# Kernel tuning notes

Hardware: AMD Instinct MI355X
Metric: run time of the kernel (lower is better)

The kernel has to match this reference:

```python
import jax, jax.numpy as jnp
import numpy as np

N = 50000      # nodes
E = 800000     # edges (before self loops)
ND = 64        # node_dim
ED = 32        # embed_dim
D = ND + 2 * ED  # 128, EGNN working feature dim


def _mlp2(x, w1, b1, w2, b2):
    return jax.nn.relu(x @ w1 + b1) @ w2 + b2


def _egnn_layer(x, pos, src, dst, nm_w1, nm_b1, nm_w2, nm_b2,
                cm_w1, cm_b1, cm_w2, cm_b2):
    # x_i = x[dst] (target), x_j = x[src] (source); aggregate at dst (PyG 'add')
    edge_vec = pos[src] - pos[dst]                                   # pos_j - pos_i, [E+N, 3]
    dist = jnp.sqrt(jnp.sum(edge_vec * edge_vec, axis=-1, keepdims=True) + 1e-8)
    h = jnp.concatenate([x[dst], x[src], dist], axis=-1)             # [E+N, 2D+1]
    edge_msg = _mlp2(h, nm_w1, nm_b1, nm_w2, nm_b2)                  # [E+N, D]
    coord_upd = _mlp2(dist, cm_w1, cm_b1, cm_w2, cm_b2) * edge_vec   # [E+N, 3]
    x_out = x + jax.ops.segment_sum(edge_msg, dst, num_segments=N)
    pos_out = pos + jax.ops.segment_sum(coord_upd, dst, num_segments=N)
    return x_out, pos_out


def setup_inputs() -> dict:
    key = jax.random.key(0)
    ks = jax.random.split(key, 24)

    def p(k, shape, scale=0.02):
        return (jax.random.normal(k, shape, jnp.float32) * scale)

    inp = {
        'x_t': jax.random.normal(ks[0], (N, ND), jnp.float32),
        'pos': jax.random.normal(ks[1], (N, 3), jnp.float32),
        'edge_index': jax.random.randint(ks[2], (2, E), 0, N, dtype=jnp.int32),
        't': jax.random.randint(ks[3], (1,), 0, 1000, dtype=jnp.int32),
        'cond_embed': jax.random.normal(ks[4], (1, ED), jnp.float32),
        # time embedding: Linear(1,32) -> ReLU -> Linear(32, ED)
        'te_w1': p(ks[5], (1, 32)), 'te_b1': jnp.zeros((32,), jnp.float32),
        'te_w2': p(ks[6], (32, ED)), 'te_b2': jnp.zeros((ED,), jnp.float32),
        # EGNN layer 1
        'l1_nm_w1': p(ks[7], (2 * D + 1, 128)), 'l1_nm_b1': jnp.zeros((128,), jnp.float32),
        'l1_nm_w2': p(ks[8], (128, D)), 'l1_nm_b2': jnp.zeros((D,), jnp.float32),
        'l1_cm_w1': p(ks[9], (1, 128)), 'l1_cm_b1': jnp.zeros((128,), jnp.float32),
        'l1_cm_w2': p(ks[10], (128, 1)), 'l1_cm_b2': jnp.zeros((1,), jnp.float32),
        # EGNN layer 2
        'l2_nm_w1': p(ks[11], (2 * D + 1, 128)), 'l2_nm_b1': jnp.zeros((128,), jnp.float32),
        'l2_nm_w2': p(ks[12], (128, D)), 'l2_nm_b2': jnp.zeros((D,), jnp.float32),
        'l2_cm_w1': p(ks[13], (1, 128)), 'l2_cm_b1': jnp.zeros((128,), jnp.float32),
        'l2_cm_w2': p(ks[14], (128, 1)), 'l2_cm_b2': jnp.zeros((1,), jnp.float32),
        # bond predictor: Linear(2D,64) -> ReLU -> Linear(64,4)
        'bp_w1': p(ks[15], (2 * D, 64)), 'bp_b1': jnp.zeros((64,), jnp.float32),
        'bp_w2': p(ks[16], (64, 4)), 'bp_b2': jnp.zeros((4,), jnp.float32),
    }
    return inp


def reference(x_t, pos, edge_index, t, cond_embed,
              te_w1, te_b1, te_w2, te_b2,
              l1_nm_w1, l1_nm_b1, l1_nm_w2, l1_nm_b2,
              l1_cm_w1, l1_cm_b1, l1_cm_w2, l1_cm_b2,
              l2_nm_w1, l2_nm_b1, l2_nm_w2, l2_nm_b2,
              l2_cm_w1, l2_cm_b1, l2_cm_w2, l2_cm_b2,
              bp_w1, bp_b1, bp_w2, bp_b2):
    n = x_t.shape[0]
    # time embedding, broadcast over nodes
    t_in = (t.reshape(-1, 1).astype(jnp.float32)) / 1000.0
    t_embed = _mlp2(t_in, te_w1, te_b1, te_w2, te_b2)            # [1, ED]
    x_input = jnp.concatenate([
        x_t,
        jnp.broadcast_to(cond_embed, (n, cond_embed.shape[-1])),
        jnp.broadcast_to(t_embed, (n, t_embed.shape[-1])),
    ], axis=1)                                                    # [N, D]

    # add self loops (appended, as in PyG add_self_loops)
    loop = jnp.arange(n, dtype=edge_index.dtype)
    src = jnp.concatenate([edge_index[0], loop])
    dst = jnp.concatenate([edge_index[1], loop])

    x1, pos1 = _egnn_layer(x_input, pos, src, dst,
                           l1_nm_w1, l1_nm_b1, l1_nm_w2, l1_nm_b2,
                           l1_cm_w1, l1_cm_b1, l1_cm_w2, l1_cm_b2)
    x2, pos2 = _egnn_layer(x1, pos1, src, dst,
                           l2_nm_w1, l2_nm_b1, l2_nm_w2, l2_nm_b2,
                           l2_cm_w1, l2_cm_b1, l2_cm_w2, l2_cm_b2)

    edge_feats = jnp.concatenate([x2[edge_index[0]], x2[edge_index[1]]], axis=1)  # [E, 2D]
    bond_logits = _mlp2(edge_feats, bp_w1, bp_b1, bp_w2, bp_b2)                   # [E, 4]
    return (x2[:, :x_t.shape[1]], bond_logits)
```

## Files before the change

### kernel.cpp

```cpp
#include <hip/hip_runtime.h>
#include <hip/hip_bf16.h>
#include <stdint.h>

typedef float  f32x4 __attribute__((ext_vector_type(4)));
typedef short  s16x8 __attribute__((ext_vector_type(8)));
typedef unsigned short u16x8 __attribute__((ext_vector_type(8)));
typedef unsigned short ushort_t;

__device__ __forceinline__ short f2bf(float f) {
  union { float f; unsigned u; } x; x.f = f;
  unsigned r = x.u + 0x7fffu + ((x.u >> 16) & 1u);
  return (short)(r >> 16);
}
__device__ __forceinline__ float bf2f(unsigned short u) {
  union { unsigned u; float f; } x; x.u = ((unsigned)u) << 16; return x.f;
}
__device__ __forceinline__ float i2f(int v) {
  union { int i; float f; } x; x.i = v; return x.f;
}
__device__ __forceinline__ int f2i(float v) {
  union { float f; int i; } x; x.f = v; return x.i;
}

__device__ __forceinline__ void pack_one(const float* W, int cols, int local, short* dst) {
  int NT = cols / 16;
  int j = local & 7, l = (local >> 3) & 63;
  int nt = (local >> 9) % NT;
  int kt = (local >> 9) / NT;
  int k = kt * 32 + ((l >> 4) * 8) + j;
  int ncol = nt * 16 + (l & 15);
  dst[local] = f2bf(W[(size_t)k * cols + ncol]);
}

__global__ __launch_bounds__(256)
void k_front(const float* __restrict__ w0, const float* __restrict__ w1,
             const float* __restrict__ w2, const float* __restrict__ w3,
             const float* __restrict__ w4, const float* __restrict__ w5,
             const float* __restrict__ w6, const float* __restrict__ w7,
             short* __restrict__ out,
             const int* __restrict__ t, const float* __restrict__ tw1,
             const float* __restrict__ tb1, const float* __restrict__ tw2,
             const float* __restrict__ tb2,
             const float* __restrict__ xt, const float* __restrict__ cond,
             ushort_t* __restrict__ X, int n,
             const int* __restrict__ edst, int E, int* __restrict__ deg,
             int nbBuild) {
  int b = blockIdx.x;
  if (b < 448) {
    int i = b * 256 + threadIdx.x;
    if (i < 98304) {
      int r = i >> 14, local = i & 16383;
      const float* W = r == 0 ? w0 : r == 1 ? w1 : r == 2 ? w2 : r == 3 ? w3 : r == 4 ? w4 : w5;
      pack_one(W, 128, local, out + r * 16384);
    } else {
      int j = i - 98304;
      int r = j >> 13, local = j & 8191;
      pack_one(r ? w7 : w6, 64, local, out + 98304 + r * 8192);
    }
    return;
  }
  b -= 448;
  if (b < nbBuild) {
    __shared__ float h[32], tembL[32];
    int j = threadIdx.x;
    if (j < 32) h[j] = fmaxf(((float)t[0] / 1000.0f) * tw1[j] + tb1[j], 0.f);
    __syncthreads();
    if (j < 32) {
      float acc = tb2[j];
      for (int k2 = 0; k2 < 32; ++k2) acc += h[k2] * tw2[k2 * 32 + j];
      tembL[j] = acc;
    }
    __syncthreads();
    int i = b * 256 + threadIdx.x;
    if (i >= n * 16) return;
    int node = i >> 4, c8 = i & 15;
    float va[8];
    if (c8 < 8)       { const float* p = &xt[(size_t)node * 64 + c8 * 8];
                        #pragma unroll
                        for (int q = 0; q < 8; ++q) va[q] = p[q]; }
    else if (c8 < 12) { const float* p = &cond[(c8 - 8) * 8];
                        #pragma unroll
                        for (int q = 0; q < 8; ++q) va[q] = p[q]; }
    else              { const float* p = &tembL[(c8 - 12) * 8];
                        #pragma unroll
                        for (int q = 0; q < 8; ++q) va[q] = p[q]; }
    u16x8 o;
    #pragma unroll
    for (int q = 0; q < 8; ++q) o[q] = f2bf(va[q]);
    *(u16x8*)&X[(size_t)node * 128 + c8 * 8] = o;
    return;
  }
  b -= nbBuild;
  int e = b * 256 + threadIdx.x;
  if (e < E) atomicAdd(&deg[edst[e]], 1);
}

__global__ void k_scan1(const int* __restrict__ deg, int* __restrict__ tmp,
                        int* __restrict__ bsum, int n) {
  __shared__ int sh[256];
  int i = blockIdx.x * 256 + threadIdx.x;
  int v = (i < n) ? deg[i] + 1 : 0;
  sh[threadIdx.x] = v; __syncthreads();
  for (int off = 1; off < 256; off <<= 1) {
    int t = (threadIdx.x >= off) ? sh[threadIdx.x - off] : 0;
    __syncthreads();
    sh[threadIdx.x] += t;
    __syncthreads();
  }
  if (i < n) tmp[i] = sh[threadIdx.x];
  if (threadIdx.x == 255) bsum[blockIdx.x] = sh[255];
}
__global__ void k_scan2(int* __restrict__ bsum, int nb) {
  __shared__ int sh[256];
  int t = threadIdx.x;
  int v = (t < nb) ? bsum[t] : 0;
  sh[t] = v; __syncthreads();
  for (int off = 1; off < 256; off <<= 1) {
    int u = (t >= off) ? sh[t - off] : 0;
    __syncthreads();
    sh[t] += u;
    __syncthreads();
  }
  if (t < nb) bsum[t] = sh[t] - v;
}
__global__ void k_scan3(const int* __restrict__ deg, const int* __restrict__ tmp,
                        const int* __restrict__ bsum, int* __restrict__ row,
                        int* __restrict__ cursor, int n) {
  int i = blockIdx.x * 256 + threadIdx.x;
  if (i < n) {
    int incl = tmp[i] + bsum[i >> 8];
    row[i + 1] = incl;
    cursor[(size_t)i * 32] = incl - (deg[i] + 1);
    if (i == 0) row[0] = 0;
  }
}

__device__ __forceinline__
void dual_body(const ushort_t* A, const short* Wp, const float* bias1,
               ushort_t* out1, ushort_t* out2, int n, int bid, short* BL) {
  const int NT = 8;
  int t = threadIdx.x, wid = t >> 6, lane = t & 63;
  int cg = lane >> 4;
  int ntiles = (n + 15) >> 4;
  int tile = bid * 4 + wid;
  bool valid = tile < ntiles;
  int r0 = (valid ? tile : 0) << 4;
  int arow = r0 + (lane & 15);
  int crow = arow < n ? arow : 0;
  const ushort_t* Ar = A + (size_t)crow * 128;
  s16x8 Af[4];
  #pragma unroll
  for (int kt = 0; kt < 4; ++kt)
    Af[kt] = *(const s16x8*)(Ar + kt * 32 + cg * 8);
  float bb[NT];
  #pragma unroll
  for (int nt = 0; nt < NT; ++nt)
    bb[nt] = bias1 ? bias1[nt * 16 + (lane & 15)] : 0.f;
  #pragma unroll
  for (int w = 0; w < 2; ++w) {
    for (int i = threadIdx.x; i < 2048; i += 256)
      ((int4*)BL)[i] = ((const int4*)Wp)[w * 2048 + i];
    __syncthreads();
    ushort_t* outp = w ? out2 : out1;
    #pragma unroll
    for (int nt = 0; nt < NT; ++nt) {
      f32x4 acc = {0.f, 0.f, 0.f, 0.f};
      #pragma unroll
      for (int kt = 0; kt < 4; ++kt) {
        s16x8 bfr = *(const s16x8*)&BL[((kt * NT + nt) * 64 + lane) * 8];
        acc = __builtin_amdgcn_mfma_f32_16x16x32_bf16(Af[kt], bfr, acc, 0, 0, 0);
      }
      int ncol = nt * 16 + (lane & 15);
      float badd = w ? 0.f : bb[nt];
      #pragma unroll
      for (int reg = 0; reg < 4; ++reg) {
        int rr = r0 + cg * 4 + reg;
        if (valid && rr < n)
          outp[(size_t)rr * 128 + ncol] = (ushort_t)f2bf(acc[reg] + badd);
      }
    }
    if (w == 0) __syncthreads();
  }
}

__global__ __launch_bounds__(256)
void k_dual_scatter(const ushort_t* __restrict__ A, const short* __restrict__ Wp,
                    const float* __restrict__ bias1,
                    ushort_t* __restrict__ out1, ushort_t* __restrict__ out2,
                    int n, int ngemm,
                    const int* __restrict__ ei, int E, int nE,
                    int* __restrict__ cursor, int4* __restrict__ csr32,
                    const float* __restrict__ pos,
                    const float* __restrict__ cw1, const float* __restrict__ cb1,
                    const float* __restrict__ cw2, const float* __restrict__ cb2) {
  __shared__ short BL[128 * 128];
  if ((int)blockIdx.x < ngemm) {
    dual_body(A, Wp, bias1, out1, out2, n, blockIdx.x, BL);
    return;
  }
  int e = (blockIdx.x - ngemm) * 256 + threadIdx.x;
  if (e >= nE) return;
  int s, d, id;
  if (e < E) { s = ei[e]; d = ei[E + e]; id = e; }
  else       { s = d = e - E; id = -1; }
  int slot = atomicAdd(&cursor[(size_t)d * 32], 1);
  float dx = pos[s*3+0] - pos[d*3+0];
  float dy = pos[s*3+1] - pos[d*3+1];
  float dz = pos[s*3+2] - pos[d*3+2];
  float dist = sqrtf(dx*dx + dy*dy + dz*dz + 1e-8f);
  float hh = cb2[0];
  #pragma unroll 4
  for (int j = 0; j < 128; ++j)
    hh += fmaxf(fmaf(dist, cw1[j], cb1[j]), 0.f) * cw2[j];
  int4 c0; c0.x = s; c0.y = d; c0.z = id; c0.w = f2i(dist);
  int4 c1; c1.x = f2i(hh * dx); c1.y = f2i(hh * dy); c1.z = f2i(hh * dz); c1.w = 0;
  csr32[(size_t)slot * 2 + 0] = c0;
  csr32[(size_t)slot * 2 + 1] = c1;
}

__global__ __launch_bounds__(256)
void k_mgemm_dual2(const ushort_t* __restrict__ A, const short* __restrict__ Wp,
                   const float* __restrict__ bias1,
                   ushort_t* __restrict__ out1, ushort_t* __restrict__ out2, int n) {
  __shared__ short BL[128 * 128];
  dual_body(A, Wp, bias1, out1, out2, n, blockIdx.x, BL);
}

__device__ __forceinline__
void mgemm_body(const ushort_t* A, const short* Wp, const float* bias,
                const ushort_t* resid, const float* degf, ushort_t* out,
                float* out64, int n, int bid, short* BL) {
  const int NT = 8;
  for (int i = threadIdx.x; i < 2048; i += 256)
    ((int4*)BL)[i] = ((const int4*)Wp)[i];
  __syncthreads();
  int t = threadIdx.x, wid = t >> 6, lane = t & 63;
  int cg = lane >> 4;
  float bb[NT];
  #pragma unroll
  for (int nt = 0; nt < NT; ++nt)
    bb[nt] = bias ? bias[nt * 16 + (lane & 15)] : 0.f;
  int ntiles = (n + 15) >> 4;
  int tile = bid * 4 + wid;
  if (tile >= ntiles) return;
  int r0 = tile << 4;
  int arow = r0 + (lane & 15);
  int crow = arow < n ? arow : 0;
  const ushort_t* Ar = A + (size_t)crow * 128;
  s16x8 Af[4];
  #pragma unroll
  for (int kt = 0; kt < 4; ++kt)
    Af[kt] = *(const s16x8*)(Ar + kt * 32 + cg * 8);
  float dsc[4];
  #pragma unroll
  for (int reg = 0; reg < 4; ++reg) {
    int rr = r0 + cg * 4 + reg;
    dsc[reg] = degf ? degf[rr < n ? rr : 0] : 1.f;
  }
  #pragma unroll
  for (int nt = 0; nt < NT; ++nt) {
    f32x4 acc = {0.f, 0.f, 0.f, 0.f};
    #pragma unroll
    for (int kt = 0; kt < 4; ++kt) {
      s16x8 bfr = *(const s16x8*)&BL[((kt * NT + nt) * 64 + lane) * 8];
      acc = __builtin_amdgcn_mfma_f32_16x16x32_bf16(Af[kt], bfr, acc, 0, 0, 0);
    }
    int ncol = nt * 16 + (lane & 15);
    #pragma unroll
    for (int reg = 0; reg < 4; ++reg) {
      int rr = r0 + cg * 4 + reg;
      if (rr < n) {
        float v = acc[reg] + dsc[reg] * bb[nt];
        if (resid) v += bf2f(resid[(size_t)rr * 128 + ncol]);
        out[(size_t)rr * 128 + ncol] = (ushort_t)f2bf(v);
        if (out64 && ncol < 64) out64[(size_t)rr * 64 + ncol] = v;
      }
    }
  }
}

__global__ __launch_bounds__(256)
void k_mgemm(const ushort_t* __restrict__ A, const short* __restrict__ Wp,
             const float* __restrict__ bias, const ushort_t* __restrict__ resid,
             const float* __restrict__ degf, ushort_t* __restrict__ out,
             float* __restrict__ out64, int n) {
  __shared__ short BL[128 * 128];
  mgemm_body(A, Wp, bias, resid, degf, out, out64, n, blockIdx.x, BL);
}

__global__ __launch_bounds__(256)
void k_post_aux(const ushort_t* __restrict__ A, const short* __restrict__ Wp,
                const float* __restrict__ bias, const ushort_t* __restrict__ resid,
                const float* __restrict__ degf, ushort_t* __restrict__ out,
                int n, int ngemm,
                const int4* __restrict__ csr32,
                int nE, const float* __restrict__ pos1, float* __restrict__ auxd) {
  __shared__ short BL[128 * 128];
  if ((int)blockIdx.x < ngemm) {
    mgemm_body(A, Wp, bias, resid, degf, out, nullptr, n, blockIdx.x, BL);
    return;
  }
  int k = (blockIdx.x - ngemm) * 256 + threadIdx.x;
  if (k >= nE) return;
  int4 c = csr32[(size_t)k * 2];
  int s = c.x, d = c.y;
  float dx = pos1[s*3+0] - pos1[d*3+0];
  float dy = pos1[s*3+1] - pos1[d*3+1];
  float dz = pos1[s*3+2] - pos1[d*3+2];
  auxd[k] = sqrtf(dx*dx + dy*dy + dz*dz + 1e-8f);
}

__global__ __launch_bounds__(256)
void k_mgemm_dual64(const ushort_t* __restrict__ A, const short* __restrict__ Wp,
                    const float* __restrict__ bias1,
                    ushort_t* __restrict__ out1, ushort_t* __restrict__ out2, int n) {
  const int COLS = 64, NT = 4;
  __shared__ short BL[2 * 128 * COLS];
  for (int i = threadIdx.x; i < 2 * 128 * COLS / 8; i += 256)
    ((int4*)BL)[i] = ((const int4*)Wp)[i];
  __syncthreads();
  int t = threadIdx.x, wid = t >> 6, lane = t & 63;
  int cg = lane >> 4;
  float bb[NT];
  #pragma unroll
  for (int nt = 0; nt < NT; ++nt)
    bb[nt] = bias1 ? bias1[nt * 16 + (lane & 15)] : 0.f;
  int ntiles = (n + 15) >> 4;
  for (int tile = blockIdx.x * 4 + wid; tile < ntiles; tile += gridDim.x * 4) {
    int r0 = tile << 4;
    int arow = r0 + (lane & 15);
    int crow = arow < n ? arow : 0;
    const ushort_t* Ar = A + (size_t)crow * 128;
    s16x8 Af[4];
    #pragma unroll
    for (int kt = 0; kt < 4; ++kt)
      Af[kt] = *(const s16x8*)(Ar + kt * 32 + cg * 8);
    #pragma unroll
    for (int w = 0; w < 2; ++w) {
      ushort_t* outp = w ? out2 : out1;
      #pragma unroll
      for (int nt = 0; nt < NT; ++nt) {
        f32x4 acc = {0.f, 0.f, 0.f, 0.f};
        #pragma unroll
        for (int kt = 0; kt < 4; ++kt) {
          s16x8 bfr = *(const s16x8*)&BL[(w * 128 * COLS / 8 + (kt * NT + nt) * 64 + lane) * 8];
          acc = __builtin_amdgcn_mfma_f32_16x16x32_bf16(Af[kt], bfr, acc, 0, 0, 0);
        }
        int ncol = nt * 16 + (lane & 15);
        float badd = w ? 0.f : bb[nt];
        #pragma unroll
        for (int reg = 0; reg < 4; ++reg) {
          int rr = r0 + cg * 4 + reg;
          if (rr < n)
            outp[(size_t)rr * COLS + ncol] = (ushort_t)f2bf(acc[reg] + badd);
        }
      }
    }
  }
}

template<bool L1>
__global__ __launch_bounds__(256)
void k_aggregate(const int* __restrict__ row, const int4* __restrict__ csr32,
                 const float* __restrict__ auxd,
                 const ushort_t* __restrict__ Pb, const ushort_t* __restrict__ Qb,
                 const float* __restrict__ w1r,
                 const float* __restrict__ posin, float* __restrict__ posout,
                 float* __restrict__ degf, ushort_t* __restrict__ Sb, int n) {
  int gw = (blockIdx.x * 256 + threadIdx.x) >> 6;
  if (gw >= n) return;
  int lane = threadIdx.x & 63;
  int half = lane >> 5, sub = lane & 31;
  int r0 = row[gw], r1 = row[gw + 1];
  int r1m1 = r1 - 1;

  ushort4 pu = *(const ushort4*)&Pb[(size_t)gw * 128 + (sub << 2)];
  float p0 = bf2f(pu.x), p1 = bf2f(pu.y), p2 = bf2f(pu.z), p3 = bf2f(pu.w);
  float4 wv = *(const float4*)&w1r[sub << 2];
  float a0 = 0.f, a1 = 0.f, a2 = 0.f, a3 = 0.f, pacc = 0.f;

  int k0 = r0 + half;
  bool any = k0 < r1;
  int kA = k0 < r1m1 ? k0 : r1m1;
  int kB = k0 + 2 < r1m1 ? k0 + 2 : r1m1;
  int4 cA = csr32[(size_t)kA * 2];
  int sB = csr32[(size_t)kB * 2].x;
  ushort4 qA = *(const ushort4*)&Qb[(size_t)cA.x * 128 + (sub << 2)];
  float dA, dB;
  float4 hA, hB;
  if (L1) { hA = *(const float4*)&csr32[(size_t)kA * 2 + 1]; dA = i2f(cA.w); }
  else    { dA = auxd[kA]; }

  for (int k = k0; k + 2 < r1; k += 2) {
    int kn4 = k + 4 < r1m1 ? k + 4 : r1m1;
    int kc2 = k + 2;
    int4 cB; cB.x = sB;
    int sC = csr32[(size_t)kn4 * 2].x;
    ushort4 qB = *(const ushort4*)&Qb[(size_t)sB * 128 + (sub << 2)];
    if (L1) {
      int4 cB2 = csr32[(size_t)kc2 * 2];
      hB = *(const float4*)&csr32[(size_t)kc2 * 2 + 1];
      dB = i2f(cB2.w);
    } else {
      dB = auxd[kc2];
    }
    a0 += fmaxf(fmaf(dA, wv.x, p0 + bf2f(qA.x)), 0.f);
    a1 += fmaxf(fmaf(dA, wv.y, p1 + bf2f(qA.y)), 0.f);
    a2 += fmaxf(fmaf(dA, wv.z, p2 + bf2f(qA.z)), 0.f);
    a3 += fmaxf(fmaf(dA, wv.w, p3 + bf2f(qA.w)), 0.f);
    if (L1 && sub < 3) pacc += (sub == 0) ? hA.x : (sub == 1) ? hA.y : hA.z;
    qA = qB; dA = dB; hA = hB; sB = sC;
  }
  if (any) {
    a0 += fmaxf(fmaf(dA, wv.x, p0 + bf2f(qA.x)), 0.f);
    a1 += fmaxf(fmaf(dA, wv.y, p1 + bf2f(qA.y)), 0.f);
    a2 += fmaxf(fmaf(dA, wv.z, p2 + bf2f(qA.z)), 0.f);
    a3 += fmaxf(fmaf(dA, wv.w, p3 + bf2f(qA.w)), 0.f);
    if (L1 && sub < 3) pacc += (sub == 0) ? hA.x : (sub == 1) ? hA.y : hA.z;
  }

  a0 += __shfl_xor(a0, 32, 64);
  a1 += __shfl_xor(a1, 32, 64);
  a2 += __shfl_xor(a2, 32, 64);
  a3 += __shfl_xor(a3, 32, 64);
  if (L1) pacc += __shfl_xor(pacc, 32, 64);

  if (half == 0) {
    ushort4 o;
    o.x = (ushort_t)f2bf(a0); o.y = (ushort_t)f2bf(a1);
    o.z = (ushort_t)f2bf(a2); o.w = (ushort_t)f2bf(a3);
    *(ushort4*)&Sb[(size_t)gw * 128 + (sub << 2)] = o;
  }
  if (L1) {
    if (lane < 3) posout[gw * 3 + lane] = posin[gw * 3 + lane] + pacc;
    if (lane == 0) degf[gw] = (float)(r1 - r0);
  }
}

__global__ __launch_bounds__(256)
void k_bond(const int4* __restrict__ csr32, int nE,
            const ushort_t* __restrict__ U, const ushort_t* __restrict__ V,
            const float* __restrict__ w2, const float* __restrict__ b2,
            float* __restrict__ out) {
  __shared__ float w2L[256];
  w2L[threadIdx.x] = w2[threadIdx.x];
  __syncthreads();
  int k = blockIdx.x * 256 + threadIdx.x;
  if (k >= nE) return;
  int4 c = csr32[(size_t)k * 2];
  int eid = c.z;
  if (eid < 0) return;
  int s = c.x, d = c.y;
  const ushort_t* Ur = U + (size_t)s * 64;
  const ushort_t* Vr = V + (size_t)d * 64;
  float l0 = b2[0], l1 = b2[1], l2 = b2[2], l3 = b2[3];
  #pragma unroll
  for (int c8 = 0; c8 < 8; ++c8) {
    u16x8 u = *(const u16x8*)(Ur + c8 * 8);
    u16x8 v = *(const u16x8*)(Vr + c8 * 8);
    #pragma unroll
    for (int j = 0; j < 8; ++j) {
      float h = fmaxf(bf2f(u[j]) + bf2f(v[j]), 0.f);
      const float* wr = &w2L[(c8 * 8 + j) * 4];
      l0 = fmaf(h, wr[0], l0);
      l1 = fmaf(h, wr[1], l1);
      l2 = fmaf(h, wr[2], l2);
      l3 = fmaf(h, wr[3], l3);
    }
  }
  float4 o = {l0, l1, l2, l3};
  *(float4*)&out[(size_t)eid * 4] = o;
}

extern "C" void kernel_launch(void* const* d_in, const int* in_sizes, int n_in,
                              void* d_out, int out_size, void* d_ws, size_t ws_size,
                              hipStream_t stream) {
  const float* x_t   = (const float*)d_in[0];
  const float* pos   = (const float*)d_in[1];
  const int*   ei    = (const int*)d_in[2];
  const int*   tt    = (const int*)d_in[3];
  const float* cond  = (const float*)d_in[4];
  const float* te_w1 = (const float*)d_in[5];
  const float* te_b1 = (const float*)d_in[6];
  const float* te_w2 = (const float*)d_in[7];
  const float* te_b2 = (const float*)d_in[8];
  const float* l1_nm_w1 = (const float*)d_in[9];
  const float* l1_nm_b1 = (const float*)d_in[10];
  const float* l1_nm_w2 = (const float*)d_in[11];
  const float* l1_nm_b2 = (const float*)d_in[12];
  const float* l1_cm_w1 = (const float*)d_in[13];
  const float* l1_cm_b1 = (const float*)d_in[14];
  const float* l1_cm_w2 = (const float*)d_in[15];
  const float* l1_cm_b2 = (const float*)d_in[16];
  const float* l2_nm_w1 = (const float*)d_in[17];
  const float* l2_nm_b1 = (const float*)d_in[18];
  const float* l2_nm_w2 = (const float*)d_in[19];
  const float* l2_nm_b2 = (const float*)d_in[20];
  const float* bp_w1 = (const float*)d_in[25];
  const float* bp_b1 = (const float*)d_in[26];
  const float* bp_w2 = (const float*)d_in[27];
  const float* bp_b2 = (const float*)d_in[28];

  int n  = in_sizes[0] / 64;
  int E_ = in_sizes[2] / 2;
  int nE = E_ + n;
  int nb = (n + 255) / 256;

  uintptr_t base = (uintptr_t)d_ws;
  size_t off = 0;
  auto alloc = [&](size_t bytes) -> void* {
    void* p = (void*)(base + off);
    off += (bytes + 255) & ~(size_t)255;
    return p;
  };
  short* pk    = (short*)alloc(114688 * 2);
  short* pk_l1_t = pk;
  short* pk_l1_2 = pk + 32768;
  short* pk_l2_t = pk + 49152;
  short* pk_l2_2 = pk + 81920;
  short* pk_bp_t = pk + 98304;
  ushort_t* X0b = (ushort_t*)alloc((size_t)n * 128 * 2);
  ushort_t* X1b = (ushort_t*)alloc((size_t)n * 128 * 2);
  ushort_t* Sb  = (ushort_t*)alloc((size_t)n * 128 * 2);
  ushort_t* Pbf = (ushort_t*)alloc((size_t)n * 128 * 2);
  ushort_t* Qbf = (ushort_t*)alloc((size_t)n * 128 * 2);
  int*   deg    = (int*)alloc((size_t)n * 4);
  int*   tmp    = (int*)alloc((size_t)n * 4);
  int*   bsum   = (int*)alloc(256 * 4);
  int*   rowp   = (int*)alloc(((size_t)n + 1) * 4);
  int*   cursor = (int*)alloc((size_t)n * 128);
  int4*  csr32  = (int4*)alloc((size_t)nE * 32);
  float* auxd   = (float*)alloc((size_t)nE * 4);
  float* degf   = (float*)alloc((size_t)n * 4);
  float* pos1   = (float*)alloc((size_t)n * 3 * 4);
  ushort_t* Ubf = Pbf;
  ushort_t* Vbf = Qbf;

  int nbBuild = (n * 16 + 255) / 256;
  int ndc = (E_ + 255) / 256;
  int nscat = (nE + 255) / 256;
  int nagg = (n + 3) / 4;
  int ngemm = (((n + 15) >> 4) + 3) / 4;

  hipMemsetAsync(deg, 0, (size_t)n * 4, stream);
  k_front<<<448 + nbBuild + ndc, 256, 0, stream>>>(
      l1_nm_w1, l1_nm_w1 + 16384, l1_nm_w2, l2_nm_w1, l2_nm_w1 + 16384, l2_nm_w2,
      bp_w1, bp_w1 + 128 * 64, pk,
      tt, te_w1, te_b1, te_w2, te_b2,
      x_t, cond, X0b, n, ei + E_, E_, deg, nbBuild);
  k_scan1<<<nb, 256, 0, stream>>>(deg, tmp, bsum, n);
  k_scan2<<<1, 256, 0, stream>>>(bsum, nb);
  k_scan3<<<nb, 256, 0, stream>>>(deg, tmp, bsum, rowp, cursor, n);

  k_dual_scatter<<<ngemm + nscat, 256, 0, stream>>>(
      X0b, pk_l1_t, l1_nm_b1, Pbf, Qbf, n, ngemm,
      ei, E_, nE, cursor, csr32,
      pos, l1_cm_w1, l1_cm_b1, l1_cm_w2, l1_cm_b2);

  k_aggregate<true><<<nagg, 256, 0, stream>>>(rowp, csr32, nullptr, Pbf, Qbf,
      l1_nm_w1 + 256 * 128, pos, pos1, degf, Sb, n);

  k_post_aux<<<ngemm + nscat, 256, 0, stream>>>(
      Sb, pk_l1_2, l1_nm_b2, X0b, degf, X1b, n, ngemm,
      csr32, nE, pos1, auxd);

  k_mgemm_dual2<<<ngemm, 256, 0, stream>>>(X1b, pk_l2_t, l2_nm_b1, Pbf, Qbf, n);
  k_aggregate<false><<<nagg, 256, 0, stream>>>(rowp, csr32, auxd, Pbf, Qbf,
      l2_nm_w1 + 256 * 128, nullptr, nullptr, nullptr, Sb, n);
  k_mgemm<<<ngemm, 256, 0, stream>>>(Sb, pk_l2_2, l2_nm_b2, X1b, degf, X0b, (float*)d_out, n);

  k_mgemm_dual64<<<ngemm, 256, 0, stream>>>(X0b, pk_bp_t, bp_b1, Ubf, Vbf, n);
  k_bond<<<nscat, 256, 0, stream>>>(csr32, nE, Ubf, Vbf,
                                    bp_w2, bp_b2, (float*)d_out + (size_t)n * 64);
}
```

Before: 283.1 us.

## Fold layer-1 output GEMM into layer-2 input weights via precomputed products

Uses linearity to precompute weight products (W2 of layer 1 times the layer-2 first-layer weight halves) and bias vectors in the front kernel. Layer-2 P/Q projections are then built from X0 projections plus the aggregated S1 times the product weights, so the materialised X1 is no longer needed. The residual, the final node output and the bond-predictor projections are fused into one final kernel. This removes a kernel launch and some full-size intermediate traffic. In exchange it adds extra GEMM phases, more workspace buffers, and extra bf16 rounding from composing the weight products.

```diff
diff --git a/kernel.cpp b/kernel.cpp
--- a/kernel.cpp
+++ b/kernel.cpp
@@ -37,7 +37,9 @@
              const float* __restrict__ w2, const float* __restrict__ w3,
              const float* __restrict__ w4, const float* __restrict__ w5,
              const float* __restrict__ w6, const float* __restrict__ w7,
-             short* __restrict__ out,
+             short* __restrict__ pk, short* __restrict__ pkprod,
+             const float* __restrict__ b21, const float* __restrict__ b22,
+             float* __restrict__ fvec,
              const int* __restrict__ t, const float* __restrict__ tw1,
              const float* __restrict__ tb1, const float* __restrict__ tw2,
              const float* __restrict__ tb2,
@@ -51,15 +53,50 @@
     if (i < 98304) {
       int r = i >> 14, local = i & 16383;
       const float* W = r == 0 ? w0 : r == 1 ? w1 : r == 2 ? w2 : r == 3 ? w3 : r == 4 ? w4 : w5;
-      pack_one(W, 128, local, out + r * 16384);
+      pack_one(W, 128, local, pk + r * 16384);
     } else {
       int j = i - 98304;
       int r = j >> 13, local = j & 8191;
-      pack_one(r ? w7 : w6, 64, local, out + 98304 + r * 8192);
+      pack_one(r ? w7 : w6, 64, local, pk + 98304 + r * 8192);
     }
     return;
   }
   b -= 448;
+  if (b < 128) {
+    int p = b >> 6;
+    int local = (b & 63) * 256 + threadIdx.x;
+    int jj = local & 7, l = (local >> 3) & 63;
+    int nt = (local >> 9) & 7, kt = (local >> 9) >> 3;
+    int k = kt * 32 + ((l >> 4) * 8) + jj;
+    int ncol = nt * 16 + (l & 15);
+    const float* W21f = w2;
+    const float* Wx = p ? (w3 + 16384) : w3;
+    float acc = 0.f;
+    #pragma unroll 4
+    for (int m = 0; m < 128; ++m)
+      acc += W21f[(size_t)k * 128 + m] * Wx[(size_t)m * 128 + ncol];
+    pkprod[p * 16384 + local] = f2bf(acc);
+    return;
+  }
+  b -= 128;
+  if (b == 0) {
+    int tid = threadIdx.x;
+    if (tid < 128) {
+      float acc = 0.f;
+      #pragma unroll 4
+      for (int k = 0; k < 128; ++k) acc += b21[k] * w3[(size_t)k * 128 + tid];
+      fvec[tid] = acc;
+      fvec[256 + tid] = b21[tid] + b22[tid];
+    } else {
+      int j = tid - 128;
+      float acc = 0.f;
+      #pragma unroll 4
+      for (int k = 0; k < 128; ++k) acc += b21[k] * w3[16384 + (size_t)k * 128 + j];
+      fvec[128 + j] = acc;
+    }
+    return;
+  }
+  b -= 1;
   if (b < nbBuild) {
     __shared__ float h[32], tembL[32];
     int j = threadIdx.x;
@@ -135,14 +172,45 @@
   }
 }
 
-__device__ __forceinline__
-void dual_body(const ushort_t* A, const short* Wp, const float* bias1,
-               ushort_t* out1, ushort_t* out2, int n, int bid, short* BL) {
+__global__ __launch_bounds__(256)
+void k_quad_scatter(const ushort_t* __restrict__ A, const short* __restrict__ pk,
+                    const float* __restrict__ bias1,
+                    ushort_t* __restrict__ P1, ushort_t* __restrict__ Q1,
+                    ushort_t* __restrict__ P2a, ushort_t* __restrict__ Q2a,
+                    int n, int nscat,
+                    const int* __restrict__ ei, int E, int nE,
+                    int* __restrict__ cursor, int4* __restrict__ csr32,
+                    const float* __restrict__ pos,
+                    const float* __restrict__ cw1, const float* __restrict__ cb1,
+                    const float* __restrict__ cw2, const float* __restrict__ cb2) {
+  __shared__ short BL[128 * 128];
+  if ((int)blockIdx.x < nscat) {
+    int e = blockIdx.x * 256 + threadIdx.x;
+    if (e >= nE) return;
+    int s, d, id;
+    if (e < E) { s = ei[e]; d = ei[E + e]; id = e; }
+    else       { s = d = e - E; id = -1; }
+    int slot = atomicAdd(&cursor[(size_t)d * 32], 1);
+    float dx = pos[s*3+0] - pos[d*3+0];
+    float dy = pos[s*3+1] - pos[d*3+1];
+    float dz = pos[s*3+2] - pos[d*3+2];
+    float dist = sqrtf(dx*dx + dy*dy + dz*dz + 1e-8f);
+    float hh = cb2[0];
+    #pragma unroll 4
+    for (int j = 0; j < 128; ++j)
+      hh += fmaxf(fmaf(dist, cw1[j], cb1[j]), 0.f) * cw2[j];
+    int4 c0; c0.x = s; c0.y = d; c0.z = id; c0.w = f2i(dist);
+    int4 c1; c1.x = f2i(hh * dx); c1.y = f2i(hh * dy); c1.z = f2i(hh * dz); c1.w = 0;
+    csr32[(size_t)slot * 2 + 0] = c0;
+    csr32[(size_t)slot * 2 + 1] = c1;
+    return;
+  }
   const int NT = 8;
+  int gb = blockIdx.x - nscat;
   int t = threadIdx.x, wid = t >> 6, lane = t & 63;
   int cg = lane >> 4;
   int ntiles = (n + 15) >> 4;
-  int tile = bid * 4 + wid;
+  int tile = gb * 4 + wid;
   bool valid = tile < ntiles;
   int r0 = (valid ? tile : 0) << 4;
   int arow = r0 + (lane & 15);
@@ -155,13 +223,15 @@
   float bb[NT];
   #pragma unroll
   for (int nt = 0; nt < NT; ++nt)
-    bb[nt] = bias1 ? bias1[nt * 16 + (lane & 15)] : 0.f;
-  #pragma unroll
-  for (int w = 0; w < 2; ++w) {
+    bb[nt] = bias1[nt * 16 + (lane & 15)];
+  const int offs[4] = {0, 2048, 6144, 8192};
+  ushort_t* outs0 = P1;
+  #pragma unroll
+  for (int ph = 0; ph < 4; ++ph) {
+    ushort_t* outp = ph == 0 ? P1 : ph == 1 ? Q1 : ph == 2 ? P2a : Q2a;
     for (int i = threadIdx.x; i < 2048; i += 256)
-      ((int4*)BL)[i] = ((const int4*)Wp)[w * 2048 + i];
-    __syncthreads();
-    ushort_t* outp = w ? out2 : out1;
+      ((int4*)BL)[i] = ((const int4*)pk)[offs[ph] + i];
+    __syncthreads();
     #pragma unroll
     for (int nt = 0; nt < NT; ++nt) {
       f32x4 acc = {0.f, 0.f, 0.f, 0.f};
@@ -171,7 +241,7 @@
         acc = __builtin_amdgcn_mfma_f32_16x16x32_bf16(Af[kt], bfr, acc, 0, 0, 0);
       }
       int ncol = nt * 16 + (lane & 15);
-      float badd = w ? 0.f : bb[nt];
+      float badd = ph == 0 ? bb[nt] : 0.f;
       #pragma unroll
       for (int reg = 0; reg < 4; ++reg) {
         int rr = r0 + cg * 4 + reg;
@@ -179,125 +249,71 @@
           outp[(size_t)rr * 128 + ncol] = (ushort_t)f2bf(acc[reg] + badd);
       }
     }
-    if (w == 0) __syncthreads();
-  }
+    __syncthreads();
+  }
+  (void)outs0;
 }
 
 __global__ __launch_bounds__(256)
-void k_dual_scatter(const ushort_t* __restrict__ A, const short* __restrict__ Wp,
-                    const float* __restrict__ bias1,
-                    ushort_t* __restrict__ out1, ushort_t* __restrict__ out2,
-                    int n, int ngemm,
-                    const int* __restrict__ ei, int E, int nE,
-                    int* __restrict__ cursor, int4* __restrict__ csr32,
-                    const float* __restrict__ pos,
-                    const float* __restrict__ cw1, const float* __restrict__ cb1,
-                    const float* __restrict__ cw2, const float* __restrict__ cb2) {
+void k_dualresid_aux(const ushort_t* __restrict__ S1, const short* __restrict__ pkprod,
+                     const float* __restrict__ fvec, const float* __restrict__ bc1,
+                     const ushort_t* __restrict__ P2a, const ushort_t* __restrict__ Q2a,
+                     const float* __restrict__ degf,
+                     ushort_t* __restrict__ P2, ushort_t* __restrict__ Q2,
+                     int n, int ngemm,
+                     const int4* __restrict__ csr32, int nE,
+                     const float* __restrict__ pos1, float* __restrict__ auxd) {
   __shared__ short BL[128 * 128];
   if ((int)blockIdx.x < ngemm) {
-    dual_body(A, Wp, bias1, out1, out2, n, blockIdx.x, BL);
-    return;
-  }
-  int e = (blockIdx.x - ngemm) * 256 + threadIdx.x;
-  if (e >= nE) return;
-  int s, d, id;
-  if (e < E) { s = ei[e]; d = ei[E + e]; id = e; }
-  else       { s = d = e - E; id = -1; }
-  int slot = atomicAdd(&cursor[(size_t)d * 32], 1);
-  float dx = pos[s*3+0] - pos[d*3+0];
-  float dy = pos[s*3+1] - pos[d*3+1];
-  float dz = pos[s*3+2] - pos[d*3+2];
-  float dist = sqrtf(dx*dx + dy*dy + dz*dz + 1e-8f);
-  float hh = cb2[0];
-  #pragma unroll 4
-  for (int j = 0; j < 128; ++j)
-    hh += fmaxf(fmaf(dist, cw1[j], cb1[j]), 0.f) * cw2[j];
-  int4 c0; c0.x = s; c0.y = d; c0.z = id; c0.w = f2i(dist);
-  int4 c1; c1.x = f2i(hh * dx); c1.y = f2i(hh * dy); c1.z = f2i(hh * dz); c1.w = 0;
-  csr32[(size_t)slot * 2 + 0] = c0;
-  csr32[(size_t)slot * 2 + 1] = c1;
-}
-
-__global__ __launch_bounds__(256)
-void k_mgemm_dual2(const ushort_t* __restrict__ A, const short* __restrict__ Wp,
-                   const float* __restrict__ bias1,
-                   ushort_t* __restrict__ out1, ushort_t* __restrict__ out2, int n) {
-  __shared__ short BL[128 * 128];
-  dual_body(A, Wp, bias1, out1, out2, n, blockIdx.x, BL);
-}
-
-__device__ __forceinline__
-void mgemm_body(const ushort_t* A, const short* Wp, const float* bias,
-                const ushort_t* resid, const float* degf, ushort_t* out,
-                float* out64, int n, int bid, short* BL) {
-  const int NT = 8;
-  for (int i = threadIdx.x; i < 2048; i += 256)
-    ((int4*)BL)[i] = ((const int4*)Wp)[i];
-  __syncthreads();
-  int t = threadIdx.x, wid = t >> 6, lane = t & 63;
-  int cg = lane >> 4;
-  float bb[NT];
-  #pragma unroll
-  for (int nt = 0; nt < NT; ++nt)
-    bb[nt] = bias ? bias[nt * 16 + (lane & 15)] : 0.f;
-  int ntiles = (n + 15) >> 4;
-  int tile = bid * 4 + wid;
-  if (tile >= ntiles) return;
-  int r0 = tile << 4;
-  int arow = r0 + (lane & 15);
-  int crow = arow < n ? arow : 0;
-  const ushort_t* Ar = A + (size_t)crow * 128;
-  s16x8 Af[4];
-  #pragma unroll
-  for (int kt = 0; kt < 4; ++kt)
-    Af[kt] = *(const s16x8*)(Ar + kt * 32 + cg * 8);
-  float dsc[4];
-  #pragma unroll
-  for (int reg = 0; reg < 4; ++reg) {
-    int rr = r0 + cg * 4 + reg;
-    dsc[reg] = degf ? degf[rr < n ? rr : 0] : 1.f;
-  }
-  #pragma unroll
-  for (int nt = 0; nt < NT; ++nt) {
-    f32x4 acc = {0.f, 0.f, 0.f, 0.f};
-    #pragma unroll
-    for (int kt = 0; kt < 4; ++kt) {
-      s16x8 bfr = *(const s16x8*)&BL[((kt * NT + nt) * 64 + lane) * 8];
-      acc = __builtin_amdgcn_mfma_f32_16x16x32_bf16(Af[kt], bfr, acc, 0, 0, 0);
-    }
-    int ncol = nt * 16 + (lane & 15);
+    const int NT = 8;
+    int t = threadIdx.x, wid = t >> 6, lane = t & 63;
+    int cg = lane >> 4;
+    int ntiles = (n + 15) >> 4;
+    int tile = blockIdx.x * 4 + wid;
+    bool valid = tile < ntiles;
+    int r0 = (valid ? tile : 0) << 4;
+    int arow = r0 + (lane & 15);
+    int crow = arow < n ? arow : 0;
+    const ushort_t* Ar = S1 + (size_t)crow * 128;
+    s16x8 Af[4];
+    #pragma unroll
+    for (int kt = 0; kt < 4; ++kt)
+      Af[kt] = *(const s16x8*)(Ar + kt * 32 + cg * 8);
+    float dsc[4];
     #pragma unroll
     for (int reg = 0; reg < 4; ++reg) {
       int rr = r0 + cg * 4 + reg;
-      if (rr < n) {
-        float v = acc[reg] + dsc[reg] * bb[nt];
-        if (resid) v += bf2f(resid[(size_t)rr * 128 + ncol]);
-        out[(size_t)rr * 128 + ncol] = (ushort_t)f2bf(v);
-        if (out64 && ncol < 64) out64[(size_t)rr * 64 + ncol] = v;
+      dsc[reg] = degf[rr < n ? rr : 0];
+    }
+    #pragma unroll
+    for (int ph = 0; ph < 2; ++ph) {
+      for (int i = threadIdx.x; i < 2048; i += 256)
+        ((int4*)BL)[i] = ((const int4*)pkprod)[ph * 2048 + i];
+      __syncthreads();
+      ushort_t* outp = ph ? Q2 : P2;
+      const ushort_t* residp = ph ? Q2a : P2a;
+      #pragma unroll
+      for (int nt = 0; nt < NT; ++nt) {
+        f32x4 acc = {0.f, 0.f, 0.f, 0.f};
+        #pragma unroll
+        for (int kt = 0; kt < 4; ++kt) {
+          s16x8 bfr = *(const s16x8*)&BL[((kt * NT + nt) * 64 + lane) * 8];
+          acc = __builtin_amdgcn_mfma_f32_16x16x32_bf16(Af[kt], bfr, acc, 0, 0, 0);
+        }
+        int ncol = nt * 16 + (lane & 15);
+        float bv = fvec[ph * 128 + ncol];
+        float bc = ph ? 0.f : bc1[ncol];
+        #pragma unroll
+        for (int reg = 0; reg < 4; ++reg) {
+          int rr = r0 + cg * 4 + reg;
+          if (valid && rr < n) {
+            float v = acc[reg] + dsc[reg] * bv + bc + bf2f(residp[(size_t)rr * 128 + ncol]);
+            outp[(size_t)rr * 128 + ncol] = (ushort_t)f2bf(v);
+          }
+        }
       }
-    }
-  }
-}
-
-__global__ __launch_bounds__(256)
-void k_mgemm(const ushort_t* __restrict__ A, const short* __restrict__ Wp,
-             const float* __restrict__ bias, const ushort_t* __restrict__ resid,
-             const float* __restrict__ degf, ushort_t* __restrict__ out,
-             float* __restrict__ out64, int n) {
-  __shared__ short BL[128 * 128];
-  mgemm_body(A, Wp, bias, resid, degf, out, out64, n, blockIdx.x, BL);
-}
-
-__global__ __launch_bounds__(256)
-void k_post_aux(const ushort_t* __restrict__ A, const short* __restrict__ Wp,
-                const float* __restrict__ bias, const ushort_t* __restrict__ resid,
-                const float* __restrict__ degf, ushort_t* __restrict__ out,
-                int n, int ngemm,
-                const int4* __restrict__ csr32,
-                int nE, const float* __restrict__ pos1, float* __restrict__ auxd) {
-  __shared__ short BL[128 * 128];
-  if ((int)blockIdx.x < ngemm) {
-    mgemm_body(A, Wp, bias, resid, degf, out, nullptr, n, blockIdx.x, BL);
+      __syncthreads();
+    }
     return;
   }
   int k = (blockIdx.x - ngemm) * 256 + threadIdx.x;
@@ -311,49 +327,95 @@
 }
 
 __global__ __launch_bounds__(256)
-void k_mgemm_dual64(const ushort_t* __restrict__ A, const short* __restrict__ Wp,
-                    const float* __restrict__ bias1,
-                    ushort_t* __restrict__ out1, ushort_t* __restrict__ out2, int n) {
-  const int COLS = 64, NT = 4;
-  __shared__ short BL[2 * 128 * COLS];
-  for (int i = threadIdx.x; i < 2 * 128 * COLS / 8; i += 256)
-    ((int4*)BL)[i] = ((const int4*)Wp)[i];
-  __syncthreads();
+void k_final(const ushort_t* __restrict__ S1, const ushort_t* __restrict__ S2,
+             const ushort_t* __restrict__ X0b, const float* __restrict__ degf,
+             const float* __restrict__ bX, const short* __restrict__ pk,
+             const float* __restrict__ bpb1,
+             float* __restrict__ out64, ushort_t* __restrict__ U, ushort_t* __restrict__ V,
+             int n) {
+  __shared__ short BL[16384];
+  __shared__ short XL[4 * 16 * 136];
+  const int NT = 8;
   int t = threadIdx.x, wid = t >> 6, lane = t & 63;
   int cg = lane >> 4;
-  float bb[NT];
-  #pragma unroll
-  for (int nt = 0; nt < NT; ++nt)
-    bb[nt] = bias1 ? bias1[nt * 16 + (lane & 15)] : 0.f;
   int ntiles = (n + 15) >> 4;
-  for (int tile = blockIdx.x * 4 + wid; tile < ntiles; tile += gridDim.x * 4) {
-    int r0 = tile << 4;
-    int arow = r0 + (lane & 15);
-    int crow = arow < n ? arow : 0;
-    const ushort_t* Ar = A + (size_t)crow * 128;
+  int tile = blockIdx.x * 4 + wid;
+  bool valid = tile < ntiles;
+  int r0 = (valid ? tile : 0) << 4;
+  int arow = r0 + (lane & 15);
+  int crow = arow < n ? arow : 0;
+  float dsc[4];
+  #pragma unroll
+  for (int reg = 0; reg < 4; ++reg) {
+    int rr = r0 + cg * 4 + reg;
+    dsc[reg] = degf[rr < n ? rr : 0];
+  }
+  f32x4 acc[NT];
+  #pragma unroll
+  for (int nt = 0; nt < NT; ++nt) acc[nt] = (f32x4){0.f, 0.f, 0.f, 0.f};
+  #pragma unroll
+  for (int ph = 0; ph < 2; ++ph) {
+    const ushort_t* Sp = ph ? S2 : S1;
+    int woff = ph ? 10240 : 4096;
+    for (int i = threadIdx.x; i < 2048; i += 256)
+      ((int4*)BL)[i] = ((const int4*)pk)[woff + i];
+    __syncthreads();
+    const ushort_t* Ar = Sp + (size_t)crow * 128;
     s16x8 Af[4];
     #pragma unroll
     for (int kt = 0; kt < 4; ++kt)
       Af[kt] = *(const s16x8*)(Ar + kt * 32 + cg * 8);
     #pragma unroll
-    for (int w = 0; w < 2; ++w) {
-      ushort_t* outp = w ? out2 : out1;
+    for (int nt = 0; nt < NT; ++nt) {
       #pragma unroll
-      for (int nt = 0; nt < NT; ++nt) {
-        f32x4 acc = {0.f, 0.f, 0.f, 0.f};
-        #pragma unroll
-        for (int kt = 0; kt < 4; ++kt) {
-          s16x8 bfr = *(const s16x8*)&BL[(w * 128 * COLS / 8 + (kt * NT + nt) * 64 + lane) * 8];
-          acc = __builtin_amdgcn_mfma_f32_16x16x32_bf16(Af[kt], bfr, acc, 0, 0, 0);
-        }
-        int ncol = nt * 16 + (lane & 15);
-        float badd = w ? 0.f : bb[nt];
-        #pragma unroll
-        for (int reg = 0; reg < 4; ++reg) {
-          int rr = r0 + cg * 4 + reg;
-          if (rr < n)
-            outp[(size_t)rr * COLS + ncol] = (ushort_t)f2bf(acc[reg] + badd);
-        }
+      for (int kt = 0; kt < 4; ++kt) {
+        s16x8 bfr = *(const s16x8*)&BL[((kt * NT + nt) * 64 + lane) * 8];
+        acc[nt] = __builtin_amdgcn_mfma_f32_16x16x32_bf16(Af[kt], bfr, acc[nt], 0, 0, 0);
+      }
+    }
+    __syncthreads();
+  }
+  int xbase = wid * 16 * 136;
+  #pragma unroll
+  for (int nt = 0; nt < NT; ++nt) {
+    int ncol = nt * 16 + (lane & 15);
+    float bxv = bX[ncol];
+    #pragma unroll
+    for (int reg = 0; reg < 4; ++reg) {
+      int rr = r0 + cg * 4 + reg;
+      float v = acc[nt][reg] + dsc[reg] * bxv;
+      if (valid && rr < n) v += bf2f(X0b[(size_t)rr * 128 + ncol]);
+      if (valid && rr < n && ncol < 64) out64[(size_t)rr * 64 + ncol] = v;
+      XL[xbase + (cg * 4 + reg) * 136 + ncol] = f2bf(v);
+    }
+  }
+  __syncthreads();
+  for (int i = threadIdx.x; i < 2048; i += 256)
+    ((int4*)BL)[i] = ((const int4*)pk)[12288 + i];
+  __syncthreads();
+  s16x8 Ax[4];
+  #pragma unroll
+  for (int kt = 0; kt < 4; ++kt)
+    Ax[kt] = *(const s16x8*)&XL[xbase + (lane & 15) * 136 + kt * 32 + cg * 8];
+  #pragma unroll
+  for (int w = 0; w < 2; ++w) {
+    ushort_t* outp = w ? V : U;
+    const short* BLc = BL + w * 8192;
+    #pragma unroll
+    for (int nt = 0; nt < 4; ++nt) {
+      f32x4 a4 = {0.f, 0.f, 0.f, 0.f};
+      #pragma unroll
+      for (int kt = 0; kt < 4; ++kt) {
+        s16x8 bfr = *(const s16x8*)&BLc[((kt * 4 + nt) * 64 + lane) * 8];
+        a4 = __builtin_amdgcn_mfma_f32_16x16x32_bf16(Ax[kt], bfr, a4, 0, 0, 0);
+      }
+      int ncol = nt * 16 + (lane & 15);
+      float badd = w ? 0.f : bpb1[ncol];
+      #pragma unroll
+      for (int reg = 0; reg < 4; ++reg) {
+        int rr = r0 + cg * 4 + reg;
+        if (valid && rr < n)
+          outp[(size_t)rr * 64 + ncol] = (ushort_t)f2bf(a4[reg] + badd);
       }
     }
   }
@@ -394,7 +456,6 @@
   for (int k = k0; k + 2 < r1; k += 2) {
     int kn4 = k + 4 < r1m1 ? k + 4 : r1m1;
     int kc2 = k + 2;
-    int4 cB; cB.x = sB;
     int sC = csr32[(size_t)kn4 * 2].x;
     ushort4 qB = *(const ushort4*)&Qb[(size_t)sB * 128 + (sub << 2)];
     if (L1) {
@@ -513,17 +574,18 @@
     off += (bytes + 255) & ~(size_t)255;
     return p;
   };
-  short* pk    = (short*)alloc(114688 * 2);
-  short* pk_l1_t = pk;
-  short* pk_l1_2 = pk + 32768;
-  short* pk_l2_t = pk + 49152;
-  short* pk_l2_2 = pk + 81920;
-  short* pk_bp_t = pk + 98304;
+  short* pk     = (short*)alloc(114688 * 2);
+  short* pkprod = (short*)alloc(32768 * 2);
+  float* fvec   = (float*)alloc(384 * 4);
   ushort_t* X0b = (ushort_t*)alloc((size_t)n * 128 * 2);
-  ushort_t* X1b = (ushort_t*)alloc((size_t)n * 128 * 2);
-  ushort_t* Sb  = (ushort_t*)alloc((size_t)n * 128 * 2);
   ushort_t* Pbf = (ushort_t*)alloc((size_t)n * 128 * 2);
   ushort_t* Qbf = (ushort_t*)alloc((size_t)n * 128 * 2);
+  ushort_t* P2a = (ushort_t*)alloc((size_t)n * 128 * 2);
+  ushort_t* Q2a = (ushort_t*)alloc((size_t)n * 128 * 2);
+  ushort_t* Sb1 = (ushort_t*)alloc((size_t)n * 128 * 2);
+  ushort_t* Sb2 = (ushort_t*)alloc((size_t)n * 128 * 2);
+  ushort_t* Ubf = (ushort_t*)alloc((size_t)n * 64 * 2);
+  ushort_t* Vbf = (ushort_t*)alloc((size_t)n * 64 * 2);
   int*   deg    = (int*)alloc((size_t)n * 4);
   int*   tmp    = (int*)alloc((size_t)n * 4);
   int*   bsum   = (int*)alloc(256 * 4);
@@ -533,8 +595,6 @@
   float* auxd   = (float*)alloc((size_t)nE * 4);
   float* degf   = (float*)alloc((size_t)n * 4);
   float* pos1   = (float*)alloc((size_t)n * 3 * 4);
-  ushort_t* Ubf = Pbf;
-  ushort_t* Vbf = Qbf;
 
   int nbBuild = (n * 16 + 255) / 256;
   int ndc = (E_ + 255) / 256;
@@ -543,33 +603,34 @@
   int ngemm = (((n + 15) >> 4) + 3) / 4;
 
   hipMemsetAsync(deg, 0, (size_t)n * 4, stream);
-  k_front<<<448 + nbBuild + ndc, 256, 0, stream>>>(
+  k_front<<<448 + 128 + 1 + nbBuild + ndc, 256, 0, stream>>>(
       l1_nm_w1, l1_nm_w1 + 16384, l1_nm_w2, l2_nm_w1, l2_nm_w1 + 16384, l2_nm_w2,
-      bp_w1, bp_w1 + 128 * 64, pk,
+      bp_w1, bp_w1 + 128 * 64, pk, pkprod,
+      l1_nm_b2, l2_nm_b2, fvec,
       tt, te_w1, te_b1, te_w2, te_b2,
       x_t, cond, X0b, n, ei + E_, E_, deg, nbBuild);
   k_scan1<<<nb, 256, 0, stream>>>(deg, tmp, bsum, n);
   k_scan2<<<1, 256, 0, stream>>>(bsum, nb);
   k_scan3<<<nb, 256, 0, stream>>>(deg, tmp, bsum, rowp, cursor, n);
 
-  k_dual_scatter<<<ngemm + nscat, 256, 0, stream>>>(
-      X0b, pk_l1_t, l1_nm_b1, Pbf, Qbf, n, ngemm,
+  k_quad_scatter<<<nscat + ngemm, 256, 0, stream>>>(
+      X0b, pk, l1_nm_b1, Pbf, Qbf, P2a, Q2a, n, nscat,
       ei, E_, nE, cursor, csr32,
       pos, l1_cm_w1, l1_cm_b1, l1_cm_w2, l1_cm_b2);
 
   k_aggregate<true><<<nagg, 256, 0, stream>>>(rowp, csr32, nullptr, Pbf, Qbf,
-      l1_nm_w1 + 256 * 128, pos, pos1, degf, Sb, n);
-
-  k_post_aux<<<ngemm + nscat, 256, 0, stream>>>(
-      Sb, pk_l1_2, l1_nm_b2, X0b, degf, X1b, n, ngemm,
+      l1_nm_w1 + 256 * 128, pos, pos1, degf, Sb1, n);
+
+  k_dualresid_aux<<<ngemm + nscat, 256, 0, stream>>>(
+      Sb1, pkprod, fvec, l2_nm_b1, P2a, Q2a, degf, Pbf, Qbf, n, ngemm,
       csr32, nE, pos1, auxd);
 
-  k_mgemm_dual2<<<ngemm, 256, 0, stream>>>(X1b, pk_l2_t, l2_nm_b1, Pbf, Qbf, n);
   k_aggregate<false><<<nagg, 256, 0, stream>>>(rowp, csr32, auxd, Pbf, Qbf,
-      l2_nm_w1 + 256 * 128, nullptr, nullptr, nullptr, Sb, n);
-  k_mgemm<<<ngemm, 256, 0, stream>>>(Sb, pk_l2_2, l2_nm_b2, X1b, degf, X0b, (float*)d_out, n);
-
-  k_mgemm_dual64<<<ngemm, 256, 0, stream>>>(X0b, pk_bp_t, bp_b1, Ubf, Vbf, n);
+      l2_nm_w1 + 256 * 128, nullptr, nullptr, nullptr, Sb2, n);
+
+  k_final<<<ngemm, 256, 0, stream>>>(Sb1, Sb2, X0b, degf, fvec + 256, pk, bp_b1,
+                                     (float*)d_out, Ubf, Vbf, n);
+
   k_bond<<<nscat, 256, 0, stream>>>(csr32, nE, Ubf, Vbf,
                                     bp_w2, bp_b2, (float*)d_out + (size_t)n * 64);
 }
```

New measurement: 299.7 us. 1.06x slower.
